# Optimization experiments

Measured on AMD Instinct MI355X. Metric: run time of the kernel, lower is better.

The kernel has to match this reference:

```python
import jax, jax.numpy as jnp
import numpy as np

D_MODEL = 1024
N_HEADS = 16
D_K = D_MODEL // N_HEADS  # 64
N_CLASSES = 32
S_LEN = 16   # synonyms per class
BATCH = 32
T_LEN = 512  # key/value sequence length


def setup_inputs() -> dict:
    key = jax.random.key(0)
    k1, k2, k3, k4, k5, k6 = jax.random.split(key, 6)
    Q = jax.random.normal(k1, (N_CLASSES, S_LEN, D_MODEL), dtype=jnp.float32)
    H = jax.random.normal(k2, (BATCH, T_LEN, D_MODEL), dtype=jnp.float32)
    ql = jax.random.normal(k3, (N_CLASSES, D_MODEL), dtype=jnp.float32)
    # torch Linear weights are (out_features, in_features), init N(0, 0.001)
    WQ_w = 0.001 * jax.random.normal(k4, (D_MODEL, D_MODEL), dtype=jnp.float32)
    WK_w = 0.001 * jax.random.normal(k5, (D_MODEL, D_MODEL), dtype=jnp.float32)
    WV_w = 0.001 * jax.random.normal(k6, (D_MODEL, D_MODEL), dtype=jnp.float32)
    return {"Q": Q, "H": H, "ql": ql, "WQ_w": WQ_w, "WK_w": WK_w, "WV_w": WV_w}


def reference(Q, H, ql, WQ_w, WK_w, WV_w):
    c, s, d = Q.shape
    b, t, _ = H.shape
    nh, dk = N_HEADS, D_K
    # projections (torch Linear: x @ W.T)
    q_s = (Q @ WQ_w.T).reshape(c, s, nh, dk).transpose(0, 2, 1, 3)   # czsh
    k_s = (H @ WK_w.T).reshape(b, t, nh, dk).transpose(0, 2, 1, 3)   # bzth
    Wql = ql @ WV_w.T                                                # ch
    Hh = H.reshape(b, t, nh, dk).transpose(0, 2, 1, 3)               # bzth
    WK = jnp.tanh(k_s)
    K = jnp.tanh(Hh)
    # scores: (b, c, z, s, t)
    scores = jnp.einsum('bzth,czsh->bczst', WK, q_s)
    attn = jax.nn.softmax(scores, axis=-1)
    # context: (b, c, z, s, h)
    context = jnp.einsum('bzth,bczst->bczsh', K, attn)
    # AvgPool3d((1, s, 1)) + squeeze(-2): mean over s -> (b, c, z, h)
    ctx = context.mean(axis=3).reshape(b, c, nh * dk)                # (b, c, d_model)
    output = jnp.einsum('bch,ch->bc', ctx, Wql)
    return output
```

## Files before the change

### kernel.cpp

```cpp
#include <hip/hip_runtime.h>
#include <hip/hip_bf16.h>
#include <math.h>

#define D_MODEL 1024
#define N_HEADS 16
#define D_K 64
#define N_CLASSES 32
#define S_LEN 16
#define BATCH 32
#define T_LEN 512

typedef __bf16 bf16_t;
typedef bf16_t bf16x8 __attribute__((ext_vector_type(8)));
typedef float f32x4 __attribute__((ext_vector_type(4)));
typedef long lx2 __attribute__((ext_vector_type(2)));

__device__ inline unsigned short f2bf(float f) {
    unsigned int u = __float_as_uint(f);
    unsigned int r = (u + 0x7FFFu + ((u >> 16) & 1u)) >> 16;
    return (unsigned short)r;
}
__device__ inline float fast_tanh(float x) {
    float e = __expf(2.0f * x);
    return (e - 1.0f) * __builtin_amdgcn_rcpf(e + 1.0f);
}
__device__ inline float4 fast_tanh4(float4 v) {
    return make_float4(fast_tanh(v.x), fast_tanh(v.y), fast_tanh(v.z), fast_tanh(v.w));
}
__device__ inline float dot4(float4 a, float4 b) {
    return a.x * b.x + a.y * b.y + a.z * b.z + a.w * b.w;
}
__device__ inline float exp2_fast(float x) {
    float r;
    asm("v_exp_f32 %0, %1" : "=v"(r) : "v"(x));
    return r;
}
__device__ inline int pack_fp8x4(float4 v) {
    int p = __builtin_amdgcn_cvt_pk_fp8_f32(v.x, v.y, 0, false);
    p = __builtin_amdgcn_cvt_pk_fp8_f32(v.z, v.w, p, true);
    return p;
}
__device__ inline bf16x8 bf8_from_f32(const float* p) {
    float4 a = *(const float4*)p;
    float4 b = *(const float4*)(p + 4);
    union { bf16x8 v; unsigned short s[8]; } u;
    u.s[0] = f2bf(a.x); u.s[1] = f2bf(a.y); u.s[2] = f2bf(a.z); u.s[3] = f2bf(a.w);
    u.s[4] = f2bf(b.x); u.s[5] = f2bf(b.y); u.s[6] = f2bf(b.z); u.s[7] = f2bf(b.w);
    return u.v;
}

__device__ inline void async16(void* lds, const void* g) {
    __builtin_amdgcn_global_load_lds(
        (const __attribute__((address_space(1))) unsigned int*)g,
        (__attribute__((address_space(3))) unsigned int*)lds, 16, 0, 0);
}

__global__ __launch_bounds__(256) void prep_kernel(
    const float* __restrict__ H, int* __restrict__ Hf8,
    const float* __restrict__ WK, int* __restrict__ WKf8,
    const float4* __restrict__ Q, ushort4* __restrict__ Qb,
    const float4* __restrict__ WQ, ushort4* __restrict__ WQb,
    const float* __restrict__ ql, const float* __restrict__ WV,
    float* __restrict__ wql)
{
    __shared__ __align__(16) char psm[25600];
    const int bid = blockIdx.x;
    const int tid = threadIdx.x;
    if (bid < 256) {
        float4 (*qls)[16] = (float4(*)[16])psm;
        float4 (*WVs)[17] = (float4(*)[17])(psm + 8192);
        const int n0 = (bid & 15) * 64;
        const int k0 = (bid >> 4) * 64;
        for (int i = tid; i < 512; i += 256)
            qls[i >> 4][i & 15] = *(const float4*)(ql + (size_t)(i >> 4) * D_MODEL + k0 + (i & 15) * 4);
        for (int i = tid; i < 1024; i += 256)
            WVs[i >> 4][i & 15] = *(const float4*)(WV + (size_t)(n0 + (i >> 4)) * D_MODEL + k0 + (i & 15) * 4);
        __syncthreads();

        const int n = tid & 63;
        const int c0 = (tid >> 6) * 8;
        float acc[8] = {};
        for (int kq = 0; kq < 16; kq++) {
            const float4 wv = WVs[n][kq];
#pragma unroll
            for (int c = 0; c < 8; c++) acc[c] += dot4(qls[c0 + c][kq], wv);
        }
#pragma unroll
        for (int c = 0; c < 8; c++)
            atomicAdd(&wql[(size_t)(c0 + c) * D_MODEL + n0 + n], acc[c]);
    } else if (bid < 4608) {
        float (*L)[260] = (float(*)[260])psm;
        int j = bid - 256;
        const float* in; int* out; float s; int jj;
        if (j < 4096) { in = H; out = Hf8; s = 1.0f; jj = j; }
        else { in = WK; out = WKf8; s = 512.0f; jj = j - 4096; }
        const int rb = jj >> 2;
        const int kb0 = (jj & 3) * 4;
        const float* base = in + (size_t)rb * 16 * 1024 + kb0 * 64;
#pragma unroll
        for (int it = 0; it < 4; it++) {
            const int idx = it * 256 + tid;
            const int row = idx >> 6;
            const int c0 = (idx & 63) * 4;
            *(float4*)&L[row][c0] = *(const float4*)(base + (size_t)row * 1024 + c0);
        }
        __syncthreads();
        const int quad = tid >> 6;
        const int l16 = (tid >> 2) & 15;
        const int kh = (tid & 3) >> 1;
        const int b0 = (tid & 1) * 4;
        const int klb = kh * 32 + quad * 8 + b0;
        int* outp = out + (size_t)jj * 1024 + tid;
#pragma unroll
        for (int p = 0; p < 4; p++) {
            float4 v = *(const float4*)&L[l16][p * 64 + klb];
            v.x *= s; v.y *= s; v.z *= s; v.w *= s;
            outp[p * 256] = pack_fp8x4(v);
        }
    } else {
        int i = (bid - 4608) * 256 + tid;
        const float4* in; ushort4* out; float s;
        if (i < 131072) { in = Q + i; out = Qb + i; s = 1.4426950408889634f; }
        else { i -= 131072; in = WQ + i; out = WQb + i; s = 1.0f; }
        float4 v = *in;
        ushort4 o;
        o.x = f2bf(v.x * s); o.y = f2bf(v.y * s); o.z = f2bf(v.z * s); o.w = f2bf(v.w * s);
        *out = o;
    }
}

__global__ __launch_bounds__(256) void gemms_kernel(
    const unsigned char* __restrict__ A8, const unsigned char* __restrict__ B8,
    unsigned short* __restrict__ wkt_b,
    const unsigned short* __restrict__ Qb, const unsigned short* __restrict__ WQb,
    unsigned short* __restrict__ qproj_b,
    const float* __restrict__ H, const float* __restrict__ wql,
    float* __restrict__ kv)
{
    __shared__ __align__(16) char smem[33280];
    const int bid = blockIdx.x;
    const int tid = threadIdx.x;
    const int wid = tid >> 6;
    const int lane = tid & 63;
    const int quad = lane >> 4;
    const int l16 = lane & 15;

    if (bid < 1024) {
        unsigned char* As = (unsigned char*)smem;
        unsigned char* Bs = (unsigned char*)smem + 16384;
        const int m0 = (bid & 127) * 128;
        const int n0 = (bid >> 7) * 128;
        const int wm = (wid >> 1) * 64;
        const int wn = (wid & 1) * 64;
        const int stA = wm >> 4;
        const int stB = wn >> 4;
        const int st = wid;
        const int cl = lane * 16;

        f32x4 acc[4][4] = {};
        const unsigned char* Ab = A8 + ((size_t)(m0 >> 4) * 16) * 1024;
        const unsigned char* Bb = B8 + ((size_t)(n0 >> 4) * 16) * 1024;

        auto stage = [&](int buf, int kb) {
            async16(&As[buf * 8192 + tid * 16],        Ab + ((size_t)st * 16 + kb) * 1024 + cl);
            async16(&As[buf * 8192 + 4096 + tid * 16], Ab + ((size_t)(st + 4) * 16 + kb) * 1024 + cl);
            async16(&Bs[buf * 8192 + tid * 16],        Bb + ((size_t)st * 16 + kb) * 1024 + cl);
            async16(&Bs[buf * 8192 + 4096 + tid * 16], Bb + ((size_t)(st + 4) * 16 + kb) * 1024 + cl);
        };

        stage(0, 0);
        __syncthreads();
        for (int kb = 0; kb < 16; kb++) {
            const int cur = kb & 1;
            if (kb < 15) stage(cur ^ 1, kb + 1);

            lx2 a8[4], b8[4];
#pragma unroll
            for (int mt = 0; mt < 4; mt++)
                a8[mt] = *(const lx2*)&As[cur * 8192 + (stA + mt) * 1024 + lane * 16];
#pragma unroll
            for (int nt = 0; nt < 4; nt++)
                b8[nt] = *(const lx2*)&Bs[cur * 8192 + (stB + nt) * 1024 + lane * 16];
#pragma unroll
            for (int mt = 0; mt < 4; mt++)
#pragma unroll
                for (int nt = 0; nt < 4; nt++) {
                    acc[mt][nt] = __builtin_amdgcn_mfma_f32_16x16x32_fp8_fp8(
                        a8[mt].x, b8[nt].x, acc[mt][nt], 0, 0, 0);
                    acc[mt][nt] = __builtin_amdgcn_mfma_f32_16x16x32_fp8_fp8(
                        a8[mt].y, b8[nt].y, acc[mt][nt], 0, 0, 0);
                }
            __syncthreads();
        }

#pragma unroll
        for (int mt = 0; mt < 4; mt++)
#pragma unroll
            for (int nt = 0; nt < 4; nt++)
#pragma unroll
                for (int r = 0; r < 4; r++) {
                    const int row = m0 + wm + mt * 16 + quad * 4 + r;
                    const int col = n0 + wn + nt * 16 + l16;
                    wkt_b[(size_t)row * 1024 + col] =
                        f2bf(fast_tanh(acc[mt][nt][r] * (1.0f / 512.0f)));
                }
    } else if (bid < 1056) {
        unsigned short* As = (unsigned short*)smem;
        unsigned short* Bs = (unsigned short*)(smem + 8192);
        const int q = bid - 1024;
        const int m0 = (q & 3) * 128;
        const int n0 = (q >> 2) * 128;
        const int wm = (wid >> 1) * 64;
        const int wn = (wid & 1) * 64;

        f32x4 acc[4][4] = {};
        const int r0 = tid >> 2;
        const int cc0 = (tid & 3) * 8;

        for (int k0 = 0; k0 < 1024; k0 += 32) {
            async16(&As[tid * 8],        Qb  + (size_t)(m0 + r0) * 1024 + k0 + cc0);
            async16(&As[2048 + tid * 8], Qb  + (size_t)(m0 + 64 + r0) * 1024 + k0 + cc0);
            async16(&Bs[tid * 8],        WQb + (size_t)(n0 + r0) * 1024 + k0 + cc0);
            async16(&Bs[2048 + tid * 8], WQb + (size_t)(n0 + 64 + r0) * 1024 + k0 + cc0);
            __syncthreads();

            bf16x8 af[4], bfr[4];
#pragma unroll
            for (int mt = 0; mt < 4; mt++)
                af[mt] = *(const bf16x8*)&As[(wm + mt * 16 + l16) * 32 + quad * 8];
#pragma unroll
            for (int nt = 0; nt < 4; nt++)
                bfr[nt] = *(const bf16x8*)&Bs[(wn + nt * 16 + l16) * 32 + quad * 8];
#pragma unroll
            for (int mt = 0; mt < 4; mt++)
#pragma unroll
                for (int nt = 0; nt < 4; nt++)
                    acc[mt][nt] = __builtin_amdgcn_mfma_f32_16x16x32_bf16(
                        af[mt], bfr[nt], acc[mt][nt], 0, 0, 0);
            __syncthreads();
        }

#pragma unroll
        for (int mt = 0; mt < 4; mt++)
#pragma unroll
            for (int nt = 0; nt < 4; nt++)
#pragma unroll
                for (int r = 0; r < 4; r++) {
                    const int row = m0 + wm + mt * 16 + quad * 4 + r;
                    const int col = n0 + wn + nt * 16 + l16;
                    qproj_b[(size_t)row * 1024 + col] = f2bf(acc[mt][nt][r]);
                }
    } else {
        unsigned short* Ks = (unsigned short*)smem;
        float* kvt = (float*)(smem + 16384);
        const int q = bid - 1056;
        const int chunk = q & 127;
        const int z = q >> 7;
        const int b = chunk >> 2;
        const int t0 = (chunk & 3) * 128;

#pragma unroll
        for (int it = 0; it < 8; it++) {
            const int idx = it * 256 + tid;
            const int row = idx >> 4;
            const int c4 = (idx & 15) * 4;
            float4 v = *(const float4*)(H + ((size_t)b * T_LEN + t0 + row) * D_MODEL + z * D_K + c4);
            v = fast_tanh4(v);
            ushort4 o;
            o.x = f2bf(v.x); o.y = f2bf(v.y); o.z = f2bf(v.z); o.w = f2bf(v.w);
            *(ushort4*)&Ks[row * 64 + c4] = o;
        }
        bf16x8 bfr[2][2];
#pragma unroll
        for (int ct = 0; ct < 2; ct++)
#pragma unroll
            for (int kh = 0; kh < 2; kh++)
                bfr[ct][kh] = bf8_from_f32(wql +
                    (size_t)(ct * 16 + l16) * D_MODEL + z * D_K + kh * 32 + quad * 8);
        __syncthreads();

        const int wt = wid * 32;
        f32x4 acc[2][2] = {};
#pragma unroll
        for (int tt = 0; tt < 2; tt++) {
            const bf16x8 a0 = *(const bf16x8*)&Ks[(wt + tt * 16 + l16) * 64 + quad * 8];
            const bf16x8 a1 = *(const bf16x8*)&Ks[(wt + tt * 16 + l16) * 64 + 32 + quad * 8];
#pragma unroll
            for (int ct = 0; ct < 2; ct++) {
                acc[tt][ct] = __builtin_amdgcn_mfma_f32_16x16x32_bf16(a0, bfr[ct][0], acc[tt][ct], 0, 0, 0);
                acc[tt][ct] = __builtin_amdgcn_mfma_f32_16x16x32_bf16(a1, bfr[ct][1], acc[tt][ct], 0, 0, 0);
            }
        }
#pragma unroll
        for (int tt = 0; tt < 2; tt++)
#pragma unroll
            for (int ct = 0; ct < 2; ct++)
#pragma unroll
                for (int r = 0; r < 4; r++)
                    kvt[(wt + tt * 16 + quad * 4 + r) * 33 + ct * 16 + l16] = acc[tt][ct][r];
        __syncthreads();

        float* outb = kv + (((size_t)b * 16 + z) * 32) * 512 + t0;
#pragma unroll
        for (int it = 0; it < 4; it++) {
            const int idx = it * 256 + tid;
            const int c = idx >> 5;
            const int tq = (idx & 31) * 4;
            float4 v = make_float4(kvt[(tq + 0) * 33 + c], kvt[(tq + 1) * 33 + c],
                                   kvt[(tq + 2) * 33 + c], kvt[(tq + 3) * 33 + c]);
            *(float4*)(outb + (size_t)c * 512 + tq) = v;
        }
    }
}

__global__ __launch_bounds__(512, 4) void attn_mfma(
    const unsigned short* __restrict__ qproj, const unsigned short* __restrict__ wkt,
    const float* __restrict__ kv, float* __restrict__ part)
{
    __shared__ unsigned short wkts[512 * 64];
    const int z = blockIdx.x;
    const int b = blockIdx.y;
    const int tid = threadIdx.x;
    const int wid = tid >> 6;
    const int lane = tid & 63;
    const int quad = lane >> 4;
    const int l16 = lane & 15;

    const unsigned short* wb = wkt + (size_t)(b * T_LEN) * D_MODEL + z * D_K;
#pragma unroll
    for (int it = 0; it < 8; it++) {
        const int chunk = it * 512 + tid;
        const int row = chunk >> 3;
        const int c = chunk & 7;
        async16(&wkts[chunk * 8], wb + (size_t)row * D_MODEL + ((c ^ (row & 7)) * 8));
    }

    bf16x8 af[4][2];
#pragma unroll
    for (int ct = 0; ct < 4; ct++)
#pragma unroll
        for (int kh = 0; kh < 2; kh++)
            af[ct][kh] = *(const bf16x8*)(qproj +
                (size_t)((wid * 4 + ct) * 16 + l16) * D_MODEL + z * D_K + kh * 32 + quad * 8);
    __syncthreads();

    float den[4][4], num[4][4];
#pragma unroll
    for (int ct = 0; ct < 4; ct++)
#pragma unroll
        for (int r = 0; r < 4; r++) { den[ct][r] = 0.f; num[ct][r] = 0.f; }

    const float* kvp = kv + (((size_t)b * 16 + z) * 32 + wid * 4) * 512 + l16;
    float kc[4];
#pragma unroll
    for (int ct = 0; ct < 4; ct++) kc[ct] = kvp[ct * 512];

    const int x0 = (quad ^ (l16 & 7)) * 8;
    const int x1 = ((quad ^ 4) ^ (l16 & 7)) * 8;
    for (int nt = 0; nt < 32; nt++) {
        float kn[4];
#pragma unroll
        for (int ct = 0; ct < 4; ct++) kn[ct] = kvp[ct * 512 + (nt + 1) * 16];
        const int rbase = (nt * 16 + l16) * 64;
        const bf16x8 b0 = *(const bf16x8*)&wkts[rbase + x0];
        const bf16x8 b1 = *(const bf16x8*)&wkts[rbase + x1];
        f32x4 a4[4];
        __builtin_amdgcn_s_setprio(1);
#pragma unroll
        for (int ct = 0; ct < 4; ct++) {
            f32x4 a = {};
            a = __builtin_amdgcn_mfma_f32_16x16x32_bf16(af[ct][0], b0, a, 0, 0, 0);
            a = __builtin_amdgcn_mfma_f32_16x16x32_bf16(af[ct][1], b1, a, 0, 0, 0);
            a4[ct] = a;
        }
        __builtin_amdgcn_s_setprio(0);
#pragma unroll
        for (int ct = 0; ct < 4; ct++)
#pragma unroll
            for (int r = 0; r < 4; r++) {
                const float e = exp2_fast(a4[ct][r]);
                den[ct][r] += e;
                num[ct][r] += e * kc[ct];
            }
#pragma unroll
        for (int ct = 0; ct < 4; ct++) kc[ct] = kn[ct];
    }

#pragma unroll
    for (int ct = 0; ct < 4; ct++) {
        float s = 0.f;
#pragma unroll
        for (int r = 0; r < 4; r++) {
            float d = den[ct][r], n = num[ct][r];
#pragma unroll
            for (int off = 1; off < 16; off <<= 1) {
                d += __shfl_xor(d, off, 64);
                n += __shfl_xor(n, off, 64);
            }
            s += n / d;
        }
        s += __shfl_xor(s, 16, 64);
        s += __shfl_xor(s, 32, 64);
        if (lane == 0)
            part[((size_t)(b * N_CLASSES) + wid * 4 + ct) * 16 + z] = s;
    }
}

__global__ __launch_bounds__(256) void attn_reduce(
    const float* __restrict__ part, float* __restrict__ out)
{
    const int i = blockIdx.x * 256 + threadIdx.x;
    const float* p = part + (size_t)i * 16;
    float s = 0.f;
#pragma unroll
    for (int zz = 0; zz < 16; zz++) s += p[zz];
    out[i] = s * (1.0f / 16.0f);
}

extern "C" void kernel_launch(void* const* d_in, const int* in_sizes, int n_in,
                              void* d_out, int out_size, void* d_ws, size_t ws_size,
                              hipStream_t stream)
{
    const float* Q  = (const float*)d_in[0];
    const float* H  = (const float*)d_in[1];
    const float* ql = (const float*)d_in[2];
    const float* WQ = (const float*)d_in[3];
    const float* WK = (const float*)d_in[4];
    const float* WV = (const float*)d_in[5];
    float* out = (float*)d_out;

    char* ws = (char*)d_ws;
    unsigned char*  Hf8     = (unsigned char*)(ws);
    unsigned short* Qb      = (unsigned short*)(ws + (size_t)25165824);
    unsigned short* WQb     = (unsigned short*)(ws + (size_t)26214400);
    unsigned short* qproj_b = (unsigned short*)(ws + (size_t)28311552);
    float*          part    = (float*)(ws + (size_t)30408704);
    float*          wqlb    = (float*)(ws + (size_t)31457280);
    unsigned short* wkt_b   = (unsigned short*)(ws + (size_t)33554432);
    float*          kv      = (float*)(ws + (size_t)67108864);
    unsigned char*  WKf8    = (unsigned char*)(ws + (size_t)100663296);

    dim3 thr(256);
    hipMemsetAsync(wqlb, 0, (size_t)N_CLASSES * D_MODEL * sizeof(float), stream);
    prep_kernel<<<dim3(6144), thr, 0, stream>>>(
        H, (int*)Hf8, WK, (int*)WKf8,
        (const float4*)Q, (ushort4*)Qb,
        (const float4*)WQ, (ushort4*)WQb,
        ql, WV, wqlb);
    gemms_kernel<<<dim3(3104), thr, 0, stream>>>(
        Hf8, WKf8, wkt_b, Qb, WQb, qproj_b, H, wqlb, kv);
    attn_mfma<<<dim3(16, 32), dim3(512), 0, stream>>>(qproj_b, wkt_b, kv, part);
    attn_reduce<<<dim3(4), thr, 0, stream>>>(part, out);
}
```

Baseline: 201.3 us.

## Enlarge FP8 GEMM tile to 256x128 with 512-thread blocks and pipeline attention loop

The fused GEMM kernel moves to 512-thread blocks. The WK FP8 GEMM now computes 256x128 tiles, so each staged B tile is reused across twice as many rows and the block count drops. The kv-projection blocks spread their work over 8 waves. The small bf16 Q projection uses only half the threads and leaves the rest idle. The attention kernel loop is software-pipelined so the exp/accumulate of one tile overlaps the MFMA of the next, at the cost of more live registers.

```diff
diff --git a/kernel.cpp b/kernel.cpp
--- a/kernel.cpp
+++ b/kernel.cpp
@@ -129,7 +129,7 @@
     }
 }
 
-__global__ __launch_bounds__(256) void gemms_kernel(
+__global__ __launch_bounds__(512) void gemms_kernel(
     const unsigned char* __restrict__ A8, const unsigned char* __restrict__ B8,
     unsigned short* __restrict__ wkt_b,
     const unsigned short* __restrict__ Qb, const unsigned short* __restrict__ WQb,
@@ -137,7 +137,7 @@
     const float* __restrict__ H, const float* __restrict__ wql,
     float* __restrict__ kv)
 {
-    __shared__ __align__(16) char smem[33280];
+    __shared__ __align__(16) char smem[49152];
     const int bid = blockIdx.x;
     const int tid = threadIdx.x;
     const int wid = tid >> 6;
@@ -145,16 +145,16 @@
     const int quad = lane >> 4;
     const int l16 = lane & 15;
 
-    if (bid < 1024) {
+    if (bid < 512) {
         unsigned char* As = (unsigned char*)smem;
-        unsigned char* Bs = (unsigned char*)smem + 16384;
-        const int m0 = (bid & 127) * 128;
-        const int n0 = (bid >> 7) * 128;
+        unsigned char* Bs = (unsigned char*)smem + 32768;
+        const int m0 = (bid & 63) * 256;
+        const int n0 = (bid >> 6) * 128;
         const int wm = (wid >> 1) * 64;
         const int wn = (wid & 1) * 64;
         const int stA = wm >> 4;
         const int stB = wn >> 4;
-        const int st = wid;
+        const int sub = tid >> 6;
         const int cl = lane * 16;
 
         f32x4 acc[4][4] = {};
@@ -162,10 +162,9 @@
         const unsigned char* Bb = B8 + ((size_t)(n0 >> 4) * 16) * 1024;
 
         auto stage = [&](int buf, int kb) {
-            async16(&As[buf * 8192 + tid * 16],        Ab + ((size_t)st * 16 + kb) * 1024 + cl);
-            async16(&As[buf * 8192 + 4096 + tid * 16], Ab + ((size_t)(st + 4) * 16 + kb) * 1024 + cl);
-            async16(&Bs[buf * 8192 + tid * 16],        Bb + ((size_t)st * 16 + kb) * 1024 + cl);
-            async16(&Bs[buf * 8192 + 4096 + tid * 16], Bb + ((size_t)(st + 4) * 16 + kb) * 1024 + cl);
+            async16(&As[buf * 16384 + sub * 1024 + cl],       Ab + ((size_t)sub * 16 + kb) * 1024 + cl);
+            async16(&As[buf * 16384 + (sub + 8) * 1024 + cl], Ab + ((size_t)(sub + 8) * 16 + kb) * 1024 + cl);
+            async16(&Bs[buf * 8192 + sub * 1024 + cl],        Bb + ((size_t)sub * 16 + kb) * 1024 + cl);
         };
 
         stage(0, 0);
@@ -177,7 +176,7 @@
             lx2 a8[4], b8[4];
 #pragma unroll
             for (int mt = 0; mt < 4; mt++)
-                a8[mt] = *(const lx2*)&As[cur * 8192 + (stA + mt) * 1024 + lane * 16];
+                a8[mt] = *(const lx2*)&As[cur * 16384 + (stA + mt) * 1024 + lane * 16];
 #pragma unroll
             for (int nt = 0; nt < 4; nt++)
                 b8[nt] = *(const lx2*)&Bs[cur * 8192 + (stB + nt) * 1024 + lane * 16];
@@ -204,10 +203,10 @@
                     wkt_b[(size_t)row * 1024 + col] =
                         f2bf(fast_tanh(acc[mt][nt][r] * (1.0f / 512.0f)));
                 }
-    } else if (bid < 1056) {
+    } else if (bid < 544) {
         unsigned short* As = (unsigned short*)smem;
         unsigned short* Bs = (unsigned short*)(smem + 8192);
-        const int q = bid - 1024;
+        const int q = bid - 512;
         const int m0 = (q & 3) * 128;
         const int n0 = (q >> 2) * 128;
         const int wm = (wid >> 1) * 64;
@@ -218,50 +217,55 @@
         const int cc0 = (tid & 3) * 8;
 
         for (int k0 = 0; k0 < 1024; k0 += 32) {
-            async16(&As[tid * 8],        Qb  + (size_t)(m0 + r0) * 1024 + k0 + cc0);
-            async16(&As[2048 + tid * 8], Qb  + (size_t)(m0 + 64 + r0) * 1024 + k0 + cc0);
-            async16(&Bs[tid * 8],        WQb + (size_t)(n0 + r0) * 1024 + k0 + cc0);
-            async16(&Bs[2048 + tid * 8], WQb + (size_t)(n0 + 64 + r0) * 1024 + k0 + cc0);
+            if (tid < 256) {
+                async16(&As[tid * 8],        Qb  + (size_t)(m0 + r0) * 1024 + k0 + cc0);
+                async16(&As[2048 + tid * 8], Qb  + (size_t)(m0 + 64 + r0) * 1024 + k0 + cc0);
+                async16(&Bs[tid * 8],        WQb + (size_t)(n0 + r0) * 1024 + k0 + cc0);
+                async16(&Bs[2048 + tid * 8], WQb + (size_t)(n0 + 64 + r0) * 1024 + k0 + cc0);
+            }
             __syncthreads();
-
-            bf16x8 af[4], bfr[4];
+            if (tid < 256) {
+                bf16x8 af[4], bfr[4];
+#pragma unroll
+                for (int mt = 0; mt < 4; mt++)
+                    af[mt] = *(const bf16x8*)&As[(wm + mt * 16 + l16) * 32 + quad * 8];
+#pragma unroll
+                for (int nt = 0; nt < 4; nt++)
+                    bfr[nt] = *(const bf16x8*)&Bs[(wn + nt * 16 + l16) * 32 + quad * 8];
+#pragma unroll
+                for (int mt = 0; mt < 4; mt++)
+#pragma unroll
+                    for (int nt = 0; nt < 4; nt++)
+                        acc[mt][nt] = __builtin_amdgcn_mfma_f32_16x16x32_bf16(
+                            af[mt], bfr[nt], acc[mt][nt], 0, 0, 0);
+            }
+            __syncthreads();
+        }
+
+        if (tid < 256) {
 #pragma unroll
             for (int mt = 0; mt < 4; mt++)
-                af[mt] = *(const bf16x8*)&As[(wm + mt * 16 + l16) * 32 + quad * 8];
-#pragma unroll
-            for (int nt = 0; nt < 4; nt++)
-                bfr[nt] = *(const bf16x8*)&Bs[(wn + nt * 16 + l16) * 32 + quad * 8];
-#pragma unroll
-            for (int mt = 0; mt < 4; mt++)
 #pragma unroll
                 for (int nt = 0; nt < 4; nt++)
-                    acc[mt][nt] = __builtin_amdgcn_mfma_f32_16x16x32_bf16(
-                        af[mt], bfr[nt], acc[mt][nt], 0, 0, 0);
-            __syncthreads();
-        }
-
-#pragma unroll
-        for (int mt = 0; mt < 4; mt++)
-#pragma unroll
-            for (int nt = 0; nt < 4; nt++)
-#pragma unroll
-                for (int r = 0; r < 4; r++) {
-                    const int row = m0 + wm + mt * 16 + quad * 4 + r;
-                    const int col = n0 + wn + nt * 16 + l16;
-                    qproj_b[(size_t)row * 1024 + col] = f2bf(acc[mt][nt][r]);
-                }
+#pragma unroll
+                    for (int r = 0; r < 4; r++) {
+                        const int row = m0 + wm + mt * 16 + quad * 4 + r;
+                        const int col = n0 + wn + nt * 16 + l16;
+                        qproj_b[(size_t)row * 1024 + col] = f2bf(acc[mt][nt][r]);
+                    }
+        }
     } else {
         unsigned short* Ks = (unsigned short*)smem;
         float* kvt = (float*)(smem + 16384);
-        const int q = bid - 1056;
+        const int q = bid - 544;
         const int chunk = q & 127;
         const int z = q >> 7;
         const int b = chunk >> 2;
         const int t0 = (chunk & 3) * 128;
 
 #pragma unroll
-        for (int it = 0; it < 8; it++) {
-            const int idx = it * 256 + tid;
+        for (int it = 0; it < 4; it++) {
+            const int idx = it * 512 + tid;
             const int row = idx >> 4;
             const int c4 = (idx & 15) * 4;
             float4 v = *(const float4*)(H + ((size_t)b * T_LEN + t0 + row) * D_MODEL + z * D_K + c4);
@@ -279,31 +283,28 @@
                     (size_t)(ct * 16 + l16) * D_MODEL + z * D_K + kh * 32 + quad * 8);
         __syncthreads();
 
-        const int wt = wid * 32;
-        f32x4 acc[2][2] = {};
-#pragma unroll
-        for (int tt = 0; tt < 2; tt++) {
-            const bf16x8 a0 = *(const bf16x8*)&Ks[(wt + tt * 16 + l16) * 64 + quad * 8];
-            const bf16x8 a1 = *(const bf16x8*)&Ks[(wt + tt * 16 + l16) * 64 + 32 + quad * 8];
+        const int wt = wid * 16;
+        f32x4 acc[2] = {};
+        {
+            const bf16x8 a0 = *(const bf16x8*)&Ks[(wt + l16) * 64 + quad * 8];
+            const bf16x8 a1 = *(const bf16x8*)&Ks[(wt + l16) * 64 + 32 + quad * 8];
 #pragma unroll
             for (int ct = 0; ct < 2; ct++) {
-                acc[tt][ct] = __builtin_amdgcn_mfma_f32_16x16x32_bf16(a0, bfr[ct][0], acc[tt][ct], 0, 0, 0);
-                acc[tt][ct] = __builtin_amdgcn_mfma_f32_16x16x32_bf16(a1, bfr[ct][1], acc[tt][ct], 0, 0, 0);
-            }
-        }
-#pragma unroll
-        for (int tt = 0; tt < 2; tt++)
-#pragma unroll
-            for (int ct = 0; ct < 2; ct++)
-#pragma unroll
-                for (int r = 0; r < 4; r++)
-                    kvt[(wt + tt * 16 + quad * 4 + r) * 33 + ct * 16 + l16] = acc[tt][ct][r];
+                acc[ct] = __builtin_amdgcn_mfma_f32_16x16x32_bf16(a0, bfr[ct][0], acc[ct], 0, 0, 0);
+                acc[ct] = __builtin_amdgcn_mfma_f32_16x16x32_bf16(a1, bfr[ct][1], acc[ct], 0, 0, 0);
+            }
+        }
+#pragma unroll
+        for (int ct = 0; ct < 2; ct++)
+#pragma unroll
+            for (int r = 0; r < 4; r++)
+                kvt[(wt + quad * 4 + r) * 33 + ct * 16 + l16] = acc[ct][r];
         __syncthreads();
 
         float* outb = kv + (((size_t)b * 16 + z) * 32) * 512 + t0;
 #pragma unroll
-        for (int it = 0; it < 4; it++) {
-            const int idx = it * 256 + tid;
+        for (int it = 0; it < 2; it++) {
+            const int idx = it * 512 + tid;
             const int c = idx >> 5;
             const int tq = (idx & 31) * 4;
             float4 v = make_float4(kvt[(tq + 0) * 33 + c], kvt[(tq + 1) * 33 + c],
@@ -351,39 +352,88 @@
         for (int r = 0; r < 4; r++) { den[ct][r] = 0.f; num[ct][r] = 0.f; }
 
     const float* kvp = kv + (((size_t)b * 16 + z) * 32 + wid * 4) * 512 + l16;
-    float kc[4];
+    float kc[4], kn[4];
 #pragma unroll
     for (int ct = 0; ct < 4; ct++) kc[ct] = kvp[ct * 512];
 
     const int x0 = (quad ^ (l16 & 7)) * 8;
     const int x1 = ((quad ^ 4) ^ (l16 & 7)) * 8;
-    for (int nt = 0; nt < 32; nt++) {
-        float kn[4];
-#pragma unroll
-        for (int ct = 0; ct < 4; ct++) kn[ct] = kvp[ct * 512 + (nt + 1) * 16];
-        const int rbase = (nt * 16 + l16) * 64;
+
+    f32x4 a4A[4], a4B[4];
+    {
+        const int rbase = l16 * 64;
         const bf16x8 b0 = *(const bf16x8*)&wkts[rbase + x0];
         const bf16x8 b1 = *(const bf16x8*)&wkts[rbase + x1];
-        f32x4 a4[4];
         __builtin_amdgcn_s_setprio(1);
 #pragma unroll
         for (int ct = 0; ct < 4; ct++) {
             f32x4 a = {};
             a = __builtin_amdgcn_mfma_f32_16x16x32_bf16(af[ct][0], b0, a, 0, 0, 0);
             a = __builtin_amdgcn_mfma_f32_16x16x32_bf16(af[ct][1], b1, a, 0, 0, 0);
-            a4[ct] = a;
+            a4A[ct] = a;
         }
         __builtin_amdgcn_s_setprio(0);
-#pragma unroll
-        for (int ct = 0; ct < 4; ct++)
-#pragma unroll
-            for (int r = 0; r < 4; r++) {
-                const float e = exp2_fast(a4[ct][r]);
-                den[ct][r] += e;
-                num[ct][r] += e * kc[ct];
-            }
-#pragma unroll
-        for (int ct = 0; ct < 4; ct++) kc[ct] = kn[ct];
+    }
+
+    for (int nt = 0; nt < 32; nt += 2) {
+        {
+            const int rb1 = ((nt + 1) * 16 + l16) * 64;
+            const bf16x8 c0 = *(const bf16x8*)&wkts[rb1 + x0];
+            const bf16x8 c1 = *(const bf16x8*)&wkts[rb1 + x1];
+#pragma unroll
+            for (int ct = 0; ct < 4; ct++) kn[ct] = kvp[ct * 512 + (nt + 1) * 16];
+#pragma unroll
+            for (int ct = 0; ct < 4; ct++)
+#pragma unroll
+                for (int r = 0; r < 4; r++) {
+                    const float e = exp2_fast(a4A[ct][r]);
+                    den[ct][r] += e;
+                    num[ct][r] += e * kc[ct];
+                }
+            __builtin_amdgcn_s_setprio(1);
+#pragma unroll
+            for (int ct = 0; ct < 4; ct++) {
+                f32x4 a = {};
+                a = __builtin_amdgcn_mfma_f32_16x16x32_bf16(af[ct][0], c0, a, 0, 0, 0);
+                a = __builtin_amdgcn_mfma_f32_16x16x32_bf16(af[ct][1], c1, a, 0, 0, 0);
+                a4B[ct] = a;
+            }
+            __builtin_amdgcn_s_setprio(0);
+#pragma unroll
+            for (int ct = 0; ct < 4; ct++) kc[ct] = kn[ct];
+        }
+        {
+            const bool more = (nt + 2) < 32;
+            bf16x8 d0 = {}, d1 = {};
+            if (more) {
+                const int rb2 = ((nt + 2) * 16 + l16) * 64;
+                d0 = *(const bf16x8*)&wkts[rb2 + x0];
+                d1 = *(const bf16x8*)&wkts[rb2 + x1];
+            }
+#pragma unroll
+            for (int ct = 0; ct < 4; ct++) kn[ct] = kvp[ct * 512 + (nt + 2) * 16];
+#pragma unroll
+            for (int ct = 0; ct < 4; ct++)
+#pragma unroll
+                for (int r = 0; r < 4; r++) {
+                    const float e = exp2_fast(a4B[ct][r]);
+                    den[ct][r] += e;
+                    num[ct][r] += e * kc[ct];
+                }
+            if (more) {
+                __builtin_amdgcn_s_setprio(1);
+#pragma unroll
+                for (int ct = 0; ct < 4; ct++) {
+                    f32x4 a = {};
+                    a = __builtin_amdgcn_mfma_f32_16x16x32_bf16(af[ct][0], d0, a, 0, 0, 0);
+                    a = __builtin_amdgcn_mfma_f32_16x16x32_bf16(af[ct][1], d1, a, 0, 0, 0);
+                    a4A[ct] = a;
+                }
+                __builtin_amdgcn_s_setprio(0);
+            }
+#pragma unroll
+            for (int ct = 0; ct < 4; ct++) kc[ct] = kn[ct];
+        }
     }
 
 #pragma unroll
@@ -447,7 +497,7 @@
         (const float4*)Q, (ushort4*)Qb,
         (const float4*)WQ, (ushort4*)WQb,
         ql, WV, wqlb);
-    gemms_kernel<<<dim3(3104), thr, 0, stream>>>(
+    gemms_kernel<<<dim3(2592), dim3(512), 0, stream>>>(
         Hf8, WKf8, wkt_b, Qb, WQb, qproj_b, H, wqlb, kv);
     attn_mfma<<<dim3(16, 32), dim3(512), 0, stream>>>(qproj_b, wkt_b, kv, part);
     attn_reduce<<<dim3(4), thr, 0, stream>>>(part, out);
```

After: 206.7 us. 2.7% more time.
